# Performance work log

Hardware: AMD Instinct MI355X
Metric: run time of the kernel (lower is better)

## Reference

```python
import jax, jax.numpy as jnp
import numpy as np

N_NODES = 50000
N_EDGES = 800000
D_IN = 128
D_OUT = 1


def setup_inputs() -> dict:
    key = jax.random.key(0)
    k1, k2, k3, k4 = jax.random.split(key, 4)
    X = jax.random.normal(k1, (N_NODES, D_IN), dtype=jnp.float32)
    edge_index = jax.random.randint(k2, (2, N_EDGES), 0, N_NODES, dtype=jnp.int64)
    # SAGEConv params: lin_l (with bias) applied to max-aggregated neighbors,
    # lin_r (no bias) applied to root/self features.
    scale = 1.0 / np.sqrt(D_IN)
    W_l = jax.random.uniform(k3, (D_OUT, D_IN), jnp.float32, -scale, scale)
    b_l = jnp.zeros((D_OUT,), jnp.float32)
    W_r = jax.random.uniform(k4, (D_OUT, D_IN), jnp.float32, -scale, scale)
    return {"X": X, "W_l": W_l, "b_l": b_l, "W_r": W_r, "edge_index": edge_index}


def reference(X, W_l, b_l, W_r, edge_index):
    # SAGEConv(aggr='max', root_weight=True, normalize=False):
    #   out_i = W_l @ max_{j in N(i)} x_j + b_l + W_r @ x_i
    src = edge_index[0]  # message sources (x_j)
    dst = edge_index[1]  # aggregation targets
    # scatter-max of gathered neighbor features; empty segments -> 0 (PyG fill)
    agg = jax.ops.segment_max(X[src], dst, num_segments=X.shape[0])  # [N, D_IN]
    agg = jnp.where(jnp.isfinite(agg), agg, jnp.zeros_like(agg))
    return agg @ W_l.T + b_l + X @ W_r.T  # [N, D_OUT]
```

## Files before the change

kernel.cpp:

```cpp
#include <hip/hip_runtime.h>

#define N_NODES 50000
#define N_EDGES 800000
#define D_IN    128
#define CAP     64

#define NBKT    782
#define BCAP    1280
#define EPT     16
#define EPB     (256 * EPT)
#define SPLIT_BLOCKS ((N_EDGES + EPB - 1) / EPB)
#define CVT_BLOCKS   (N_NODES / 8)


__device__ __forceinline__ unsigned int f32_to_bf16_rn(float f) {
    unsigned int u = __float_as_uint(f);
    u += 0x7fffu + ((u >> 16) & 1u);
    return u >> 16;
}

__global__ __launch_bounds__(256) void k_zero(int* __restrict__ gctr)
{
    int i = blockIdx.x * 256 + threadIdx.x;
    if (i < NBKT) gctr[i] = 0;
}

__global__ __launch_bounds__(256) void k_split_cvt(
    const int*   __restrict__ src,
    const int*   __restrict__ dst,
    int*         __restrict__ gctr,
    unsigned int* __restrict__ staging,
    const float* __restrict__ X,
    const float* __restrict__ W_r,
    const float* __restrict__ b_l,
    unsigned short* __restrict__ Xh,
    float*       __restrict__ selfdot)
{
    int b = blockIdx.x;
    if (b < SPLIT_BLOCKS) {
        __shared__ int hist[NBKT];
        __shared__ int base[NBKT];
        int tid = threadIdx.x;
        for (int i = tid; i < NBKT; i += 256) hist[i] = 0;
        __syncthreads();

        int t[EPT], s[EPT], bk[EPT];
        bool ok[EPT];
        const int4* d4 = (const int4*)dst;
        const int4* s4 = (const int4*)src;
        int q0 = b * (EPB / 4) + tid;
#pragma unroll
        for (int k = 0; k < 4; ++k) {
            int q = q0 + (k << 8);
            bool v = (q * 4) < N_EDGES;
            int qc = v ? q : 0;
            int4 dv = d4[qc];
            int4 sv = s4[qc];
            t[k*4+0] = dv.x; t[k*4+1] = dv.y; t[k*4+2] = dv.z; t[k*4+3] = dv.w;
            s[k*4+0] = sv.x; s[k*4+1] = sv.y; s[k*4+2] = sv.z; s[k*4+3] = sv.w;
            ok[k*4+0] = ok[k*4+1] = ok[k*4+2] = ok[k*4+3] = v;
        }
#pragma unroll
        for (int k = 0; k < EPT; ++k) {
            bk[k] = t[k] >> 6;
            if (ok[k]) atomicAdd(&hist[bk[k]], 1);
        }
        __syncthreads();
        for (int i = tid; i < NBKT; i += 256) {
            int h = hist[i];
            base[i] = h ? atomicAdd(&gctr[i], h) : 0;
            hist[i] = 0;
        }
        __syncthreads();
#pragma unroll
        for (int k = 0; k < EPT; ++k) {
            if (ok[k]) {
                int pos = base[bk[k]] + atomicAdd(&hist[bk[k]], 1);
                if (pos < BCAP)
                    staging[(size_t)bk[k] * BCAP + pos] =
                        ((unsigned int)(t[k] & 63) << 16) | (unsigned int)s[k];
            }
        }
        return;
    }
    int wave = ((b - SPLIT_BLOCKS) * 256 + threadIdx.x) >> 6;
    int lane = threadIdx.x & 63;
    int half = lane >> 5;
    int sub  = lane & 31;
    int row  = wave * 2 + half;
    if (row >= N_NODES) return;

    float4 x = ((const float4*)(X + (size_t)row * D_IN))[sub];
    unsigned int p0 = (f32_to_bf16_rn(x.y) << 16) | f32_to_bf16_rn(x.x);
    unsigned int p1 = (f32_to_bf16_rn(x.w) << 16) | f32_to_bf16_rn(x.z);
    ((uint2*)Xh)[row * 32 + sub] = make_uint2(p0, p1);

    float4 wr = ((const float4*)W_r)[sub];
    float acc = x.x * wr.x + x.y * wr.y + x.z * wr.z + x.w * wr.w;
#pragma unroll
    for (int off = 16; off; off >>= 1)
        acc += __shfl_down(acc, off, 32);
    if (sub == 0)
        selfdot[row] = acc + b_l[0];
}

__global__ __launch_bounds__(256) void k_build(
    const unsigned int* __restrict__ staging,
    const int*   __restrict__ gctr,
    int*         __restrict__ cnt,
    unsigned short* __restrict__ sorted16)
{
    __shared__ __align__(16) unsigned short lbuf[64 * CAP];
    __shared__ int lcnt[64];
    int b   = blockIdx.x;
    int tid = threadIdx.x;
    if (tid < 64) lcnt[tid] = 0;
    __syncthreads();

    int count = gctr[b];
    if (count > BCAP) count = BCAP;
    for (int i = tid; i < count; i += 256) {
        unsigned int rec = staging[(size_t)b * BCAP + i];
        int nlo = rec >> 16;
        int pos = atomicAdd(&lcnt[nlo], 1);
        if (pos < CAP)
            lbuf[nlo * CAP + pos] = (unsigned short)(rec & 0xffffu);
    }
    __syncthreads();

    int nodebase = b << 6;
    if (tid < 64) {
        int node = nodebase + tid;
        if (node < N_NODES) {
            int c = lcnt[tid];
            cnt[node] = c < CAP ? c : CAP;
        }
    }
    int nrows = N_NODES - nodebase;
    if (nrows > 64) nrows = 64;
    int tot128 = nrows * (CAP / 8);
    const int4* lb128 = (const int4*)lbuf;
    int4* out128 = (int4*)(sorted16 + (size_t)nodebase * CAP);
    for (int i = tid; i < tot128; i += 256)
        out128[i] = lb128[i];
}

#define GLOAD(uu, ss)  uu = Xu[((unsigned)(ss) << 6) | (unsigned)lane];
#define GMAX(mm, uu)                                                  \
    {                                                                 \
        (mm).x = fmaxf((mm).x, __uint_as_float((uu) << 16));          \
        (mm).y = fmaxf((mm).y, __uint_as_float((uu) & 0xffff0000u));  \
    }
#define GATHER(mm, ss)                                                \
    { unsigned int u_; GLOAD(u_, ss) GMAX(mm, u_) }

__global__ __launch_bounds__(256) void k_agg(
    const unsigned short* __restrict__ Xh,
    const int*   __restrict__ cnt,
    const unsigned short* __restrict__ sorted16,
    const float* __restrict__ W_l,
    const float* __restrict__ selfdot,
    float*       __restrict__ out)
{
    int wave = (blockIdx.x * 256 + threadIdx.x) >> 6;
    int lane = threadIdx.x & 63;
    if (wave >= N_NODES) return;

    int n = cnt[wave];
    int sid = (int)sorted16[wave * CAP + lane];
    if (n > CAP) n = CAP;

    float2 wl = ((const float2*)W_l)[lane];
    float sd  = selfdot[wave];

    const unsigned int* Xu = (const unsigned int*)Xh;
    float2 m[8];
#pragma unroll
    for (int k = 0; k < 8; ++k) m[k] = make_float2(-INFINITY, -INFINITY);

    int i = 0;
    for (; i + 16 <= n; i += 16) {
        int sr[16];
#pragma unroll
        for (int k = 0; k < 16; ++k) sr[k] = __shfl(sid, i + k);
        unsigned int u[16];
#pragma unroll
        for (int k = 0; k < 16; ++k) GLOAD(u[k], sr[k])
#pragma unroll
        for (int k = 0; k < 16; ++k) GMAX(m[k & 7], u[k])
    }
    if (i + 8 <= n) {
        int sr[8];
#pragma unroll
        for (int k = 0; k < 8; ++k) sr[k] = __shfl(sid, i + k);
        unsigned int u[8];
#pragma unroll
        for (int k = 0; k < 8; ++k) GLOAD(u[k], sr[k])
#pragma unroll
        for (int k = 0; k < 8; ++k) GMAX(m[k], u[k])
        i += 8;
    }
    if (i + 4 <= n) {
        int s0 = __shfl(sid, i + 0), s1 = __shfl(sid, i + 1);
        int s2 = __shfl(sid, i + 2), s3 = __shfl(sid, i + 3);
        GATHER(m[0], s0) GATHER(m[1], s1) GATHER(m[2], s2) GATHER(m[3], s3)
        i += 4;
    }
    if (i + 2 <= n) {
        int s0 = __shfl(sid, i + 0), s1 = __shfl(sid, i + 1);
        GATHER(m[0], s0) GATHER(m[1], s1)
        i += 2;
    }
    if (i < n) {
        int s0 = __shfl(sid, i);
        GATHER(m[0], s0)
    }
#pragma unroll
    for (int k = 4; k; k >>= 1)
#pragma unroll
        for (int j = 0; j < k; ++j) {
            m[j].x = fmaxf(m[j].x, m[j + k].x);
            m[j].y = fmaxf(m[j].y, m[j + k].y);
        }
    if (n == 0) { m[0].x = 0.0f; m[0].y = 0.0f; }

    float acc = m[0].x * wl.x + m[0].y * wl.y;
#pragma unroll
    for (int off = 32; off; off >>= 1)
        acc += __shfl_down(acc, off);
    if (lane == 0)
        out[wave] = acc + sd;
}

extern "C" void kernel_launch(void* const* d_in, const int* in_sizes, int n_in,
                              void* d_out, int out_size, void* d_ws, size_t ws_size,
                              hipStream_t stream)
{
    const float* X   = (const float*)d_in[0];
    const float* W_l = (const float*)d_in[1];
    const float* b_l = (const float*)d_in[2];
    const float* W_r = (const float*)d_in[3];
    const int*   ei  = (const int*)d_in[4];
    const int*   src = ei;
    const int*   dst = ei + N_EDGES;

    int* gctr = (int*)d_ws;
    unsigned int* staging = (unsigned int*)(gctr + 1024);
    int* cnt = (int*)(staging + (size_t)NBKT * BCAP);
    unsigned short* sorted16 = (unsigned short*)(cnt + N_NODES);
    unsigned short* Xh = sorted16 + (size_t)N_NODES * CAP;
    float* selfdot = (float*)(Xh + (size_t)N_NODES * D_IN);
    float* out = (float*)d_out;

    k_zero<<<(NBKT + 255) / 256, 256, 0, stream>>>(gctr);
    k_split_cvt<<<SPLIT_BLOCKS + CVT_BLOCKS, 256, 0, stream>>>(
        src, dst, gctr, staging, X, W_r, b_l, Xh, selfdot);
    k_build<<<NBKT, 256, 0, stream>>>(staging, gctr, cnt, sorted16);
    k_agg<<<(N_NODES * 64 + 255) / 256, 256, 0, stream>>>(
        Xh, cnt, sorted16, W_l, selfdot, out);
}
```

Before: 62.32 us.

## Fuse bucket build and max-aggregation into one kernel using LDS neighbor lists

Merges the per-bucket build kernel and the aggregation kernel into one launch. Each 1024-thread block sorts its bucket's edges into LDS, then 16 waves each aggregate 4 nodes by reading neighbor ids straight from LDS. This removes the global write and re-read of the sorted index array and counts, plus one launch. In exchange the grid shrinks to 782 large blocks, which cuts parallelism for latency hiding, and the per-wave loop over 4 nodes serializes the gather work.

```diff
diff --git a/kernel.cpp b/kernel.cpp
--- a/kernel.cpp
+++ b/kernel.cpp
@@ -104,13 +104,24 @@
         selfdot[row] = acc + b_l[0];
 }
 
-__global__ __launch_bounds__(256) void k_build(
+#define GLOAD(uu, ss)  uu = Xu[((unsigned)(ss) << 6) | (unsigned)lane];
+#define GMAX(mm, uu)                                                  \
+    {                                                                 \
+        (mm).x = fmaxf((mm).x, __uint_as_float((uu) << 16));          \
+        (mm).y = fmaxf((mm).y, __uint_as_float((uu) & 0xffff0000u));  \
+    }
+#define GATHER(mm, ss)                                                \
+    { unsigned int u_; GLOAD(u_, ss) GMAX(mm, u_) }
+
+__global__ __launch_bounds__(1024, 8) void k_bagg(
     const unsigned int* __restrict__ staging,
     const int*   __restrict__ gctr,
-    int*         __restrict__ cnt,
-    unsigned short* __restrict__ sorted16)
-{
-    __shared__ __align__(16) unsigned short lbuf[64 * CAP];
+    const unsigned short* __restrict__ Xh,
+    const float* __restrict__ W_l,
+    const float* __restrict__ selfdot,
+    float*       __restrict__ out)
+{
+    __shared__ unsigned short lbuf[64 * CAP];
     __shared__ int lcnt[64];
     int b   = blockIdx.x;
     int tid = threadIdx.x;
@@ -119,7 +130,7 @@
 
     int count = gctr[b];
     if (count > BCAP) count = BCAP;
-    for (int i = tid; i < count; i += 256) {
+    for (int i = tid; i < count; i += 1024) {
         unsigned int rec = staging[(size_t)b * BCAP + i];
         int nlo = rec >> 16;
         int pos = atomicAdd(&lcnt[nlo], 1);
@@ -128,108 +139,76 @@
     }
     __syncthreads();
 
+    int wid  = tid >> 6;
+    int lane = tid & 63;
+    float2 wl = ((const float2*)W_l)[lane];
+    const unsigned int* Xu = (const unsigned int*)Xh;
     int nodebase = b << 6;
-    if (tid < 64) {
-        int node = nodebase + tid;
-        if (node < N_NODES) {
-            int c = lcnt[tid];
-            cnt[node] = c < CAP ? c : CAP;
-        }
-    }
-    int nrows = N_NODES - nodebase;
-    if (nrows > 64) nrows = 64;
-    int tot128 = nrows * (CAP / 8);
-    const int4* lb128 = (const int4*)lbuf;
-    int4* out128 = (int4*)(sorted16 + (size_t)nodebase * CAP);
-    for (int i = tid; i < tot128; i += 256)
-        out128[i] = lb128[i];
-}
-
-#define GLOAD(uu, ss)  uu = Xu[((unsigned)(ss) << 6) | (unsigned)lane];
-#define GMAX(mm, uu)                                                  \
-    {                                                                 \
-        (mm).x = fmaxf((mm).x, __uint_as_float((uu) << 16));          \
-        (mm).y = fmaxf((mm).y, __uint_as_float((uu) & 0xffff0000u));  \
-    }
-#define GATHER(mm, ss)                                                \
-    { unsigned int u_; GLOAD(u_, ss) GMAX(mm, u_) }
-
-__global__ __launch_bounds__(256) void k_agg(
-    const unsigned short* __restrict__ Xh,
-    const int*   __restrict__ cnt,
-    const unsigned short* __restrict__ sorted16,
-    const float* __restrict__ W_l,
-    const float* __restrict__ selfdot,
-    float*       __restrict__ out)
-{
-    int wave = (blockIdx.x * 256 + threadIdx.x) >> 6;
-    int lane = threadIdx.x & 63;
-    if (wave >= N_NODES) return;
-
-    int n = cnt[wave];
-    int sid = (int)sorted16[wave * CAP + lane];
-    if (n > CAP) n = CAP;
-
-    float2 wl = ((const float2*)W_l)[lane];
-    float sd  = selfdot[wave];
-
-    const unsigned int* Xu = (const unsigned int*)Xh;
-    float2 m[8];
-#pragma unroll
-    for (int k = 0; k < 8; ++k) m[k] = make_float2(-INFINITY, -INFINITY);
-
-    int i = 0;
-    for (; i + 16 <= n; i += 16) {
-        int sr[16];
-#pragma unroll
-        for (int k = 0; k < 16; ++k) sr[k] = __shfl(sid, i + k);
-        unsigned int u[16];
-#pragma unroll
-        for (int k = 0; k < 16; ++k) GLOAD(u[k], sr[k])
-#pragma unroll
-        for (int k = 0; k < 16; ++k) GMAX(m[k & 7], u[k])
-    }
-    if (i + 8 <= n) {
-        int sr[8];
-#pragma unroll
-        for (int k = 0; k < 8; ++k) sr[k] = __shfl(sid, i + k);
-        unsigned int u[8];
-#pragma unroll
-        for (int k = 0; k < 8; ++k) GLOAD(u[k], sr[k])
-#pragma unroll
-        for (int k = 0; k < 8; ++k) GMAX(m[k], u[k])
-        i += 8;
-    }
-    if (i + 4 <= n) {
-        int s0 = __shfl(sid, i + 0), s1 = __shfl(sid, i + 1);
-        int s2 = __shfl(sid, i + 2), s3 = __shfl(sid, i + 3);
-        GATHER(m[0], s0) GATHER(m[1], s1) GATHER(m[2], s2) GATHER(m[3], s3)
-        i += 4;
-    }
-    if (i + 2 <= n) {
-        int s0 = __shfl(sid, i + 0), s1 = __shfl(sid, i + 1);
-        GATHER(m[0], s0) GATHER(m[1], s1)
-        i += 2;
-    }
-    if (i < n) {
-        int s0 = __shfl(sid, i);
-        GATHER(m[0], s0)
-    }
-#pragma unroll
-    for (int k = 4; k; k >>= 1)
-#pragma unroll
-        for (int j = 0; j < k; ++j) {
-            m[j].x = fmaxf(m[j].x, m[j + k].x);
-            m[j].y = fmaxf(m[j].y, m[j + k].y);
-        }
-    if (n == 0) { m[0].x = 0.0f; m[0].y = 0.0f; }
-
-    float acc = m[0].x * wl.x + m[0].y * wl.y;
-#pragma unroll
-    for (int off = 32; off; off >>= 1)
-        acc += __shfl_down(acc, off);
-    if (lane == 0)
-        out[wave] = acc + sd;
+
+#pragma unroll
+    for (int j = 0; j < 4; ++j) {
+        int li   = (wid << 2) + j;
+        int node = nodebase + li;
+        if (node >= N_NODES) continue;
+        float sd = selfdot[node];
+        int n = lcnt[li];
+        if (n > CAP) n = CAP;
+        const unsigned short* seg = &lbuf[li * CAP];
+
+        float2 m[8];
+#pragma unroll
+        for (int k = 0; k < 8; ++k) m[k] = make_float2(-INFINITY, -INFINITY);
+
+        int i = 0;
+        for (; i + 16 <= n; i += 16) {
+            int sr[16];
+#pragma unroll
+            for (int k = 0; k < 16; ++k) sr[k] = seg[i + k];
+            unsigned int u[16];
+#pragma unroll
+            for (int k = 0; k < 16; ++k) GLOAD(u[k], sr[k])
+#pragma unroll
+            for (int k = 0; k < 16; ++k) GMAX(m[k & 7], u[k])
+        }
+        if (i + 8 <= n) {
+            int sr[8];
+#pragma unroll
+            for (int k = 0; k < 8; ++k) sr[k] = seg[i + k];
+            unsigned int u[8];
+#pragma unroll
+            for (int k = 0; k < 8; ++k) GLOAD(u[k], sr[k])
+#pragma unroll
+            for (int k = 0; k < 8; ++k) GMAX(m[k], u[k])
+            i += 8;
+        }
+        if (i + 4 <= n) {
+            GATHER(m[0], seg[i + 0]) GATHER(m[1], seg[i + 1])
+            GATHER(m[2], seg[i + 2]) GATHER(m[3], seg[i + 3])
+            i += 4;
+        }
+        if (i + 2 <= n) {
+            GATHER(m[0], seg[i + 0]) GATHER(m[1], seg[i + 1])
+            i += 2;
+        }
+        if (i < n) {
+            GATHER(m[0], seg[i])
+        }
+#pragma unroll
+        for (int k = 4; k; k >>= 1)
+#pragma unroll
+            for (int q = 0; q < k; ++q) {
+                m[q].x = fmaxf(m[q].x, m[q + k].x);
+                m[q].y = fmaxf(m[q].y, m[q + k].y);
+            }
+        if (n == 0) { m[0].x = 0.0f; m[0].y = 0.0f; }
+
+        float acc = m[0].x * wl.x + m[0].y * wl.y;
+#pragma unroll
+        for (int off = 32; off; off >>= 1)
+            acc += __shfl_down(acc, off);
+        if (lane == 0)
+            out[node] = acc + sd;
+    }
 }
 
 extern "C" void kernel_launch(void* const* d_in, const int* in_sizes, int n_in,
@@ -246,16 +225,12 @@
 
     int* gctr = (int*)d_ws;
     unsigned int* staging = (unsigned int*)(gctr + 1024);
-    int* cnt = (int*)(staging + (size_t)NBKT * BCAP);
-    unsigned short* sorted16 = (unsigned short*)(cnt + N_NODES);
-    unsigned short* Xh = sorted16 + (size_t)N_NODES * CAP;
+    unsigned short* Xh = (unsigned short*)(staging + (size_t)NBKT * BCAP);
     float* selfdot = (float*)(Xh + (size_t)N_NODES * D_IN);
     float* out = (float*)d_out;
 
     k_zero<<<(NBKT + 255) / 256, 256, 0, stream>>>(gctr);
     k_split_cvt<<<SPLIT_BLOCKS + CVT_BLOCKS, 256, 0, stream>>>(
         src, dst, gctr, staging, X, W_r, b_l, Xh, selfdot);
-    k_build<<<NBKT, 256, 0, stream>>>(staging, gctr, cnt, sorted16);
-    k_agg<<<(N_NODES * 64 + 255) / 256, 256, 0, stream>>>(
-        Xh, cnt, sorted16, W_l, selfdot, out);
-}
+    k_bagg<<<NBKT, 1024, 0, stream>>>(staging, gctr, Xh, W_l, selfdot, out);
+}
```

Measured after the change: 57.01 us. -8.5%, faster.

## Slice bf16 features into four column slices for cache-local neighbor gathers

Applied to the files above, without the earlier changes.

Stores the bf16 copy of X as four 32-column slices, each contiguous across all nodes, so that each gather block touches only a 3.2MB working set. A new gather kernel processes 64 destination nodes per block for one slice, with four neighbors per wave instruction at 64B per row. It writes per-slice partial dot products that a small reduce kernel sums with the self term. The intent is better L2 hit rate on random gathers, at the cost of an extra launch, a partial buffer round-trip and 16-lane segments that are only partly used.

```diff
diff --git a/kernel.cpp b/kernel.cpp
--- a/kernel.cpp
+++ b/kernel.cpp
@@ -11,6 +11,8 @@
 #define EPB     (256 * EPT)
 #define SPLIT_BLOCKS ((N_EDGES + EPB - 1) / EPB)
 #define CVT_BLOCKS   (N_NODES / 8)
+
+#define NSLC    4
 
 
 __device__ __forceinline__ unsigned int f32_to_bf16_rn(float f) {
@@ -33,7 +35,7 @@
     const float* __restrict__ X,
     const float* __restrict__ W_r,
     const float* __restrict__ b_l,
-    unsigned short* __restrict__ Xh,
+    unsigned int* __restrict__ Xs,
     float*       __restrict__ selfdot)
 {
     int b = blockIdx.x;
@@ -93,13 +95,15 @@
     float4 x = ((const float4*)(X + (size_t)row * D_IN))[sub];
     unsigned int p0 = (f32_to_bf16_rn(x.y) << 16) | f32_to_bf16_rn(x.x);
     unsigned int p1 = (f32_to_bf16_rn(x.w) << 16) | f32_to_bf16_rn(x.z);
-    ((uint2*)Xh)[row * 32 + sub] = make_uint2(p0, p1);
+    int slice = sub >> 3;
+    int off   = sub & 7;
+    ((uint2*)Xs)[((size_t)slice * N_NODES + row) * 8 + off] = make_uint2(p0, p1);
 
     float4 wr = ((const float4*)W_r)[sub];
     float acc = x.x * wr.x + x.y * wr.y + x.z * wr.z + x.w * wr.w;
 #pragma unroll
-    for (int off = 16; off; off >>= 1)
-        acc += __shfl_down(acc, off, 32);
+    for (int off2 = 16; off2; off2 >>= 1)
+        acc += __shfl_down(acc, off2, 32);
     if (sub == 0)
         selfdot[row] = acc + b_l[0];
 }
@@ -145,91 +149,112 @@
         out128[i] = lb128[i];
 }
 
-#define GLOAD(uu, ss)  uu = Xu[((unsigned)(ss) << 6) | (unsigned)lane];
-#define GMAX(mm, uu)                                                  \
+#define SMAX(mm, uu)                                                  \
     {                                                                 \
         (mm).x = fmaxf((mm).x, __uint_as_float((uu) << 16));          \
         (mm).y = fmaxf((mm).y, __uint_as_float((uu) & 0xffff0000u));  \
     }
-#define GATHER(mm, ss)                                                \
-    { unsigned int u_; GLOAD(u_, ss) GMAX(mm, u_) }
-
-__global__ __launch_bounds__(256) void k_agg(
-    const unsigned short* __restrict__ Xh,
+
+__global__ __launch_bounds__(256) void k_sgather(
+    const unsigned short* __restrict__ sorted16,
     const int*   __restrict__ cnt,
-    const unsigned short* __restrict__ sorted16,
+    const unsigned int* __restrict__ Xs,
     const float* __restrict__ W_l,
+    float*       __restrict__ partial)
+{
+    __shared__ __align__(16) unsigned short lids[64 * CAP];
+    __shared__ int lcnt[64];
+    int slice = blockIdx.x & 3;
+    int bkt   = blockIdx.x >> 2;
+    int tid   = threadIdx.x;
+    int nodebase = bkt << 6;
+
+    const int4* sids = (const int4*)(sorted16 + (size_t)nodebase * CAP);
+    int4* dids = (int4*)lids;
+    dids[tid]       = sids[tid];
+    dids[tid + 256] = sids[tid + 256];
+    if (tid < 64) {
+        int node = nodebase + tid;
+        lcnt[tid] = (node < N_NODES) ? cnt[node] : 0;
+    }
+    __syncthreads();
+
+    int wid  = tid >> 6;
+    int lane = tid & 63;
+    int grp  = lane >> 4;
+    int d    = lane & 15;
+    float2 wl = ((const float2*)W_l)[slice * 16 + d];
+    unsigned sliceBase = (unsigned)slice * (N_NODES * 16);
+
+#pragma unroll
+    for (int j = 0; j < 16; ++j) {
+        int li   = (wid << 4) + j;
+        int node = nodebase + li;
+        if (node >= N_NODES) break;
+        int n = lcnt[li];
+        const unsigned short* seg = &lids[li * CAP];
+
+        float2 m0 = make_float2(-INFINITY, -INFINITY);
+        float2 m1 = m0, m2 = m0, m3 = m0;
+
+        int i = 0;
+        for (; i + 16 <= n; i += 16) {
+            int id0 = seg[i +      grp];
+            int id1 = seg[i + 4  + grp];
+            int id2 = seg[i + 8  + grp];
+            int id3 = seg[i + 12 + grp];
+            unsigned u0 = Xs[sliceBase + ((unsigned)id0 << 4) + d];
+            unsigned u1 = Xs[sliceBase + ((unsigned)id1 << 4) + d];
+            unsigned u2 = Xs[sliceBase + ((unsigned)id2 << 4) + d];
+            unsigned u3 = Xs[sliceBase + ((unsigned)id3 << 4) + d];
+            SMAX(m0, u0) SMAX(m1, u1) SMAX(m2, u2) SMAX(m3, u3)
+        }
+        if (i + 8 <= n) {
+            int id0 = seg[i + grp];
+            int id1 = seg[i + 4 + grp];
+            unsigned u0 = Xs[sliceBase + ((unsigned)id0 << 4) + d];
+            unsigned u1 = Xs[sliceBase + ((unsigned)id1 << 4) + d];
+            SMAX(m0, u0) SMAX(m1, u1)
+            i += 8;
+        }
+        if (i + 4 <= n) {
+            int id0 = seg[i + grp];
+            unsigned u0 = Xs[sliceBase + ((unsigned)id0 << 4) + d];
+            SMAX(m0, u0)
+            i += 4;
+        }
+        if (i < n) {
+            bool v = (i + grp) < n;
+            int idt = v ? (int)seg[i + grp] : 0;
+            unsigned ut = v ? Xs[sliceBase + ((unsigned)idt << 4) + d]
+                            : 0xFF7FFF7Fu;
+            SMAX(m0, ut)
+        }
+        m0.x = fmaxf(fmaxf(m0.x, m1.x), fmaxf(m2.x, m3.x));
+        m0.y = fmaxf(fmaxf(m0.y, m1.y), fmaxf(m2.y, m3.y));
+        m0.x = fmaxf(m0.x, __shfl_xor(m0.x, 16));
+        m0.y = fmaxf(m0.y, __shfl_xor(m0.y, 16));
+        m0.x = fmaxf(m0.x, __shfl_xor(m0.x, 32));
+        m0.y = fmaxf(m0.y, __shfl_xor(m0.y, 32));
+
+        float p = m0.x * wl.x + m0.y * wl.y;
+#pragma unroll
+        for (int off = 8; off; off >>= 1)
+            p += __shfl_down(p, off);
+        if (lane == 0)
+            partial[(size_t)slice * N_NODES + node] = (n > 0) ? p : 0.0f;
+    }
+}
+
+__global__ __launch_bounds__(256) void k_reduce(
+    const float* __restrict__ partial,
     const float* __restrict__ selfdot,
     float*       __restrict__ out)
 {
-    int wave = (blockIdx.x * 256 + threadIdx.x) >> 6;
-    int lane = threadIdx.x & 63;
-    if (wave >= N_NODES) return;
-
-    int n = cnt[wave];
-    int sid = (int)sorted16[wave * CAP + lane];
-    if (n > CAP) n = CAP;
-
-    float2 wl = ((const float2*)W_l)[lane];
-    float sd  = selfdot[wave];
-
-    const unsigned int* Xu = (const unsigned int*)Xh;
-    float2 m[8];
-#pragma unroll
-    for (int k = 0; k < 8; ++k) m[k] = make_float2(-INFINITY, -INFINITY);
-
-    int i = 0;
-    for (; i + 16 <= n; i += 16) {
-        int sr[16];
-#pragma unroll
-        for (int k = 0; k < 16; ++k) sr[k] = __shfl(sid, i + k);
-        unsigned int u[16];
-#pragma unroll
-        for (int k = 0; k < 16; ++k) GLOAD(u[k], sr[k])
-#pragma unroll
-        for (int k = 0; k < 16; ++k) GMAX(m[k & 7], u[k])
-    }
-    if (i + 8 <= n) {
-        int sr[8];
-#pragma unroll
-        for (int k = 0; k < 8; ++k) sr[k] = __shfl(sid, i + k);
-        unsigned int u[8];
-#pragma unroll
-        for (int k = 0; k < 8; ++k) GLOAD(u[k], sr[k])
-#pragma unroll
-        for (int k = 0; k < 8; ++k) GMAX(m[k], u[k])
-        i += 8;
-    }
-    if (i + 4 <= n) {
-        int s0 = __shfl(sid, i + 0), s1 = __shfl(sid, i + 1);
-        int s2 = __shfl(sid, i + 2), s3 = __shfl(sid, i + 3);
-        GATHER(m[0], s0) GATHER(m[1], s1) GATHER(m[2], s2) GATHER(m[3], s3)
-        i += 4;
-    }
-    if (i + 2 <= n) {
-        int s0 = __shfl(sid, i + 0), s1 = __shfl(sid, i + 1);
-        GATHER(m[0], s0) GATHER(m[1], s1)
-        i += 2;
-    }
-    if (i < n) {
-        int s0 = __shfl(sid, i);
-        GATHER(m[0], s0)
-    }
-#pragma unroll
-    for (int k = 4; k; k >>= 1)
-#pragma unroll
-        for (int j = 0; j < k; ++j) {
-            m[j].x = fmaxf(m[j].x, m[j + k].x);
-            m[j].y = fmaxf(m[j].y, m[j + k].y);
-        }
-    if (n == 0) { m[0].x = 0.0f; m[0].y = 0.0f; }
-
-    float acc = m[0].x * wl.x + m[0].y * wl.y;
-#pragma unroll
-    for (int off = 32; off; off >>= 1)
-        acc += __shfl_down(acc, off);
-    if (lane == 0)
-        out[wave] = acc + sd;
+    int i = blockIdx.x * 256 + threadIdx.x;
+    if (i < N_NODES)
+        out[i] = partial[i] + partial[N_NODES + i] + partial[2 * N_NODES + i]
+               + partial[3 * N_NODES + i] + selfdot[i];
 }
 
 extern "C" void kernel_launch(void* const* d_in, const int* in_sizes, int n_in,
@@ -248,14 +273,15 @@
     unsigned int* staging = (unsigned int*)(gctr + 1024);
     int* cnt = (int*)(staging + (size_t)NBKT * BCAP);
     unsigned short* sorted16 = (unsigned short*)(cnt + N_NODES);
-    unsigned short* Xh = sorted16 + (size_t)N_NODES * CAP;
-    float* selfdot = (float*)(Xh + (size_t)N_NODES * D_IN);
+    unsigned int* Xs = (unsigned int*)(sorted16 + (size_t)N_NODES * CAP);
+    float* selfdot = (float*)(Xs + (size_t)NSLC * N_NODES * 16);
+    float* partial = selfdot + N_NODES;
     float* out = (float*)d_out;
 
     k_zero<<<(NBKT + 255) / 256, 256, 0, stream>>>(gctr);
     k_split_cvt<<<SPLIT_BLOCKS + CVT_BLOCKS, 256, 0, stream>>>(
-        src, dst, gctr, staging, X, W_r, b_l, Xh, selfdot);
+        src, dst, gctr, staging, X, W_r, b_l, Xs, selfdot);
     k_build<<<NBKT, 256, 0, stream>>>(staging, gctr, cnt, sorted16);
-    k_agg<<<(N_NODES * 64 + 255) / 256, 256, 0, stream>>>(
-        Xh, cnt, sorted16, W_l, selfdot, out);
-}
+    k_sgather<<<NBKT * NSLC, 256, 0, stream>>>(sorted16, cnt, Xs, W_l, partial);
+    k_reduce<<<(N_NODES + 255) / 256, 256, 0, stream>>>(partial, selfdot, out);
+}
```

Measured after the change: 75.80 us. 1.22x slower.
